# Performance work log

Measured on AMD Instinct MI355X. Metric: run time of the kernel, lower is better.

Reference implementation:

```python
import jax, jax.numpy as jnp
import numpy as np

N = 50000      # nodes
E = 400000     # edges
HID = 128      # hidden size
H = 8          # heads
HS = HID // H  # head size = 16
TN = 8         # node types
R = 8          # relation (edge) types
L = 2          # layers
OUT = 128
EPS = 1e-5
SQRT_D = float(np.sqrt(HS))


def setup_inputs() -> dict:
    key = jax.random.key(0)
    ks = jax.random.split(key, 12)
    s = 1.0 / np.sqrt(HID)
    sh = 1.0 / np.sqrt(HS)
    return {
        "x": jax.random.normal(ks[0], (N, HID), jnp.float32),
        "edge_index": jax.random.randint(ks[1], (2, E), 0, N, dtype=jnp.int32),
        "ntype": jax.random.randint(ks[2], (N,), 0, TN, dtype=jnp.int32),
        "etype": jax.random.randint(ks[3], (E,), 0, R, dtype=jnp.int32),
        "Wk": jax.random.normal(ks[4], (L, TN, HID, HID), jnp.float32) * s,
        "Wq": jax.random.normal(ks[5], (L, TN, HID, HID), jnp.float32) * s,
        "Wv": jax.random.normal(ks[6], (L, TN, HID, HID), jnp.float32) * s,
        "Wa": jax.random.normal(ks[7], (L, TN, HID, HID), jnp.float32) * s,
        "pri": jnp.ones((L, H, R), jnp.float32),
        "Watt": jax.random.normal(ks[8], (L, H, R, HS, HS), jnp.float32) * sh,
        "Wmsg": jax.random.normal(ks[9], (L, H, R, HS, HS), jnp.float32) * sh,
        "skip": jnp.ones((L, TN), jnp.float32),
        "ln_g": jnp.ones((L, HID), jnp.float32),
        "ln_b": jnp.zeros((L, HID), jnp.float32),
        "Wff": jax.random.normal(ks[10], (HID, OUT), jnp.float32) * s,
        "bff": jnp.zeros((OUT,), jnp.float32),
    }


def typed_linear(x, types, W):
    """x:(M,din), types:(M,), W:(T,din,dout) -> (M,dout); y = x @ W[type]."""
    out = jnp.zeros((x.shape[0], W.shape[-1]), x.dtype)
    for t in range(W.shape[0]):
        out = out + jnp.where((types == t)[:, None], x @ W[t], 0.0)
    return out


def rel_apply(h, etype, W):
    """h:(E,H,hs), etype:(E,), W:(H,R,hs,hs) -> (E,H,hs); per-head, per-relation linear."""
    out = jnp.zeros_like(h)
    for r in range(W.shape[1]):
        out = out + jnp.where((etype == r)[:, None, None],
                              jnp.einsum('ehi,hio->eho', h, W[:, r]), 0.0)
    return out


def gt_layer(x, src, dst, ntype, etype, Wk, Wq, Wv, Wa, pri, Watt, Wmsg, skip, g, b):
    n = x.shape[0]
    k = typed_linear(x, ntype, Wk).reshape(n, H, HS)
    q = typed_linear(x, ntype, Wq).reshape(n, H, HS)
    v = typed_linear(x, ntype, Wv).reshape(n, H, HS)
    k_j, q_i, v_j = k[src], q[dst], v[src]          # (E,H,hs)
    kw = rel_apply(k_j, etype, Watt)                # relation-specific key transform
    a = (kw * q_i).sum(-1) * pri[:, etype].T / SQRT_D  # (E,H)
    # scatter softmax over destination nodes
    amax = jax.ops.segment_max(a, dst, num_segments=n)
    ex = jnp.exp(a - amax[dst])
    den = jax.ops.segment_sum(ex, dst, num_segments=n)
    alpha = ex / (den[dst] + 1e-16)
    m = rel_apply(v_j, etype, Wmsg)                 # relation-specific message
    agg = jax.ops.segment_sum(alpha[..., None] * m, dst, num_segments=n)
    out = jax.nn.silu(typed_linear(agg.reshape(n, HID), ntype, Wa))
    al = jax.nn.sigmoid(skip[ntype])[:, None]
    out = out * al + x * (1.0 - al)                 # gated residual (in==hid)
    mu = out.mean(-1, keepdims=True)
    var = ((out - mu) ** 2).mean(-1, keepdims=True)
    return (out - mu) / jnp.sqrt(var + EPS) * g + b


def reference(x, edge_index, ntype, etype, Wk, Wq, Wv, Wa, pri, Watt, Wmsg,
              skip, ln_g, ln_b, Wff, bff):
    src, dst = edge_index[0], edge_index[1]
    emb = x
    for l in range(L):
        emb = gt_layer(emb, src, dst, ntype, etype, Wk[l], Wq[l], Wv[l], Wa[l],
                       pri[l], Watt[l], Wmsg[l], skip[l], ln_g[l], ln_b[l])
    return emb @ Wff + bff
```

## Files before the change

kernel.cpp:

```cpp
#include <hip/hip_runtime.h>
#include <hip/hip_bf16.h>
#include <math.h>

#define N_NODES 50000
#define N_EDGES 400000
#define HID 128
#define NH 8
#define HS 16
#define TN 8
#define NR 8
#define TILE 32
#define MAXTILES 1571
#define PERM_SZ (MAXTILES * TILE)
#define SCAN_BLKS ((N_NODES + 255) / 256)
#define NB 3125
#define TPBMAX 26
#define CAP 288

typedef __attribute__((ext_vector_type(8))) short bf16x8;
typedef __attribute__((ext_vector_type(4))) float f32x4;

__device__ __forceinline__ unsigned short f2bf(float f) {
    __hip_bfloat16 h = __float2bfloat16(f);
    return *reinterpret_cast<unsigned short*>(&h);
}
__device__ __forceinline__ float bf2f(unsigned short u) {
    return __uint_as_float((unsigned)u << 16);
}

__global__ void hist_kernel(const int* __restrict__ ntype, int* __restrict__ cnt) {
    __shared__ int l[TN];
    if (threadIdx.x < TN) l[threadIdx.x] = 0;
    __syncthreads();
    int i = blockIdx.x * 256 + threadIdx.x;
    if (i < N_NODES) atomicAdd(&l[ntype[i]], 1);
    __syncthreads();
    if (threadIdx.x < TN) atomicAdd(&cnt[threadIdx.x], l[threadIdx.x]);
}
__global__ void scan_kernel(const int* __restrict__ cnt, int* __restrict__ cursor) {
    if (threadIdx.x == 0 && blockIdx.x == 0) {
        int acc = 0;
        for (int t = 0; t < TN; ++t) {
            cursor[t] = acc;
            acc += ((cnt[t] + TILE - 1) / TILE) * TILE;
        }
    }
}
__global__ void scatter_kernel(const int* __restrict__ ntype, int* __restrict__ cursor,
                               int* __restrict__ perm) {
    __shared__ int lcnt[TN], lbase[TN];
    if (threadIdx.x < TN) lcnt[threadIdx.x] = 0;
    __syncthreads();
    int i = blockIdx.x * 256 + threadIdx.x;
    int t = 0, off = 0;
    if (i < N_NODES) {
        t = ntype[i];
        off = atomicAdd(&lcnt[t], 1);
    }
    __syncthreads();
    if (threadIdx.x < TN)
        lbase[threadIdx.x] = atomicAdd(&cursor[threadIdx.x], lcnt[threadIdx.x]);
    __syncthreads();
    if (i < N_NODES) perm[lbase[t] + off] = i;
}

__global__ void hist_dst_kernel(const int* __restrict__ dst, int* __restrict__ cnt) {
    int e = blockIdx.x * 256 + threadIdx.x;
    if (e < N_EDGES) atomicAdd(&cnt[dst[e]], 1);
}
__global__ void scan_block_kernel(const int* __restrict__ cnt, int* __restrict__ excl,
                                  int* __restrict__ bsum) {
    __shared__ int s[256];
    int tid = threadIdx.x;
    int i = blockIdx.x * 256 + tid;
    int v = (i < N_NODES) ? cnt[i] : 0;
    s[tid] = v;
    __syncthreads();
    for (int off = 1; off < 256; off <<= 1) {
        int t = (tid >= off) ? s[tid - off] : 0;
        __syncthreads();
        s[tid] += t;
        __syncthreads();
    }
    if (i < N_NODES) excl[i] = s[tid] - v;
    if (tid == 255) bsum[blockIdx.x] = s[255];
}
__global__ void scan_top_kernel(int* __restrict__ bsum) {
    __shared__ int s[256];
    int tid = threadIdx.x;
    int v = (tid < SCAN_BLKS) ? bsum[tid] : 0;
    s[tid] = v;
    __syncthreads();
    for (int off = 1; off < 256; off <<= 1) {
        int t = (tid >= off) ? s[tid - off] : 0;
        __syncthreads();
        s[tid] += t;
        __syncthreads();
    }
    if (tid < SCAN_BLKS) bsum[tid] = s[tid] - v;
}
__global__ void scan_add_kernel(int* __restrict__ excl, const int* __restrict__ bsum,
                                int* __restrict__ cursor) {
    int i = blockIdx.x * 256 + threadIdx.x;
    if (i < N_NODES) {
        int v = excl[i] + bsum[blockIdx.x];
        excl[i] = v;
        cursor[i] = v;
    }
}
__global__ void csr_scatter_kernel(const int* __restrict__ src, const int* __restrict__ dst,
                                   const int* __restrict__ etype, int* __restrict__ cur_dst,
                                   int* __restrict__ csr_sd, int* __restrict__ csr_et) {
    int e = blockIdx.x * 256 + threadIdx.x;
    if (e < N_EDGES) {
        int p = atomicAdd(&cur_dst[dst[e]], 1);
        csr_sd[p] = src[e] | (dst[e] << 16);
        csr_et[p] = etype[e];
    }
}

__global__ void btile_build(const int* __restrict__ row_ptr,
                            const int* __restrict__ csr_sd, const int* __restrict__ csr_et,
                            int* __restrict__ btile_sd, int* __restrict__ btile_lp,
                            int* __restrict__ btile_r, int* __restrict__ ntb) {
    int b = blockIdx.x;
    int lane = threadIdx.x;
    int p0 = row_ptr[b * 16];
    int p1 = (b == NB - 1) ? N_EDGES : row_ptr[b * 16 + 16];
    int cnt = 0;
    if (lane < 8) {
        for (int p = p0; p < p1; ++p) cnt += (csr_et[p] == lane);
    }
    int tiles = (cnt + 15) >> 4;
    int pre = 0, total = 0;
    for (int k = 0; k < 8; ++k) {
        int tk = __shfl(tiles, k);
        if (k < lane) pre += tk;
        total += tk;
    }
    if (lane == 0) ntb[b] = total;
    if (lane < 8) {
        int tbase = b * TPBMAX + pre;
        for (int t = 0; t < tiles; ++t) btile_r[tbase + t] = lane;
        int off = 0;
        for (int p = p0; p < p1; ++p) {
            if (csr_et[p] == lane) {
                int idx = (tbase + (off >> 4)) * 16 + (off & 15);
                btile_sd[idx] = csr_sd[p];
                btile_lp[idx] = p - p0;
                ++off;
            }
        }
        for (; off < tiles * 16; ++off) {
            int idx = (tbase + (off >> 4)) * 16 + (off & 15);
            btile_sd[idx] = 0;
            btile_lp[idx] = CAP;
        }
    }
}

__global__ void wconv_kernel(const float* __restrict__ W, unsigned short* __restrict__ out) {
    int mat = blockIdx.x >> 3, seg = blockIdx.x & 7;
    const float* w = W + (size_t)mat * HID * HID;
    unsigned short* o = out + (size_t)mat * HID * HID;
#pragma unroll
    for (int c = 0; c < 8; ++c) {
        int idx = seg * 2048 + c * 256 + threadIdx.x;
        int i = idx >> 7, j = idx & 127;
        o[j * HID + i] = f2bf(w[idx]);
    }
}
__global__ void wsmall_conv(const float* __restrict__ W, const float* __restrict__ pri,
                            unsigned short* __restrict__ out) {
    int blk = blockIdx.x;
    int tid = threadIdx.x;
    int i = tid >> 4, o = tid & 15;
    float s = pri ? pri[blk] * 0.25f : 1.f;
    out[blk * 256 + o * 16 + i] = f2bf(W[blk * 256 + i * 16 + o] * s);
}

__global__ __launch_bounds__(256) void gemm3_mfma(
    const float* __restrict__ x, const int* __restrict__ perm, const int* __restrict__ ntype,
    const unsigned short* __restrict__ WkT, const unsigned short* __restrict__ WqT,
    const unsigned short* __restrict__ WvT,
    unsigned short* __restrict__ Kb, unsigned short* __restrict__ Qb,
    unsigned short* __restrict__ Vb) {
    __shared__ unsigned short xs[TILE][HID + 8];
    __shared__ int nodes[TILE];
    int tid = threadIdx.x;
    if (tid < TILE) nodes[tid] = perm[blockIdx.x * TILE + tid];
    __syncthreads();
    if (nodes[0] < 0) return;
    int t = ntype[nodes[0]];
#pragma unroll
    for (int c = 0; c < 4; ++c) {
        int v = tid + c * 256;
        int ns = v >> 5, ii = (v & 31) * 4;
        int node = nodes[ns];
        float4 val = (node >= 0) ? *(const float4*)(x + (size_t)node * HID + ii)
                                 : make_float4(0.f, 0.f, 0.f, 0.f);
        uint2 pk;
        pk.x = (unsigned)f2bf(val.x) | ((unsigned)f2bf(val.y) << 16);
        pk.y = (unsigned)f2bf(val.z) | ((unsigned)f2bf(val.w) << 16);
        *(uint2*)&xs[ns][ii] = pk;
    }
    __syncthreads();
    int wv = tid >> 6, lane = tid & 63;
    int lrow = lane & 15, lk = lane >> 4;
    bf16x8 af[2][4];
#pragma unroll
    for (int rt = 0; rt < 2; ++rt)
#pragma unroll
        for (int kk = 0; kk < 4; ++kk)
            af[rt][kk] = *(const bf16x8*)&xs[rt * 16 + lrow][kk * 32 + lk * 8];
    size_t woff = (size_t)t * HID * HID + (size_t)lrow * HID + lk * 8;
#pragma unroll
    for (int pp = 0; pp < 6; ++pp) {
        int p = wv * 6 + pp;
        int mat = p >> 3, ct = p & 7;
        const unsigned short* wb =
            (mat == 0 ? WkT : (mat == 1 ? WqT : WvT)) + woff + (size_t)ct * 16 * HID;
        unsigned short* ob = (mat == 0) ? Kb : (mat == 1 ? Qb : Vb);
        f32x4 a0 = {0.f, 0.f, 0.f, 0.f}, a1 = {0.f, 0.f, 0.f, 0.f};
#pragma unroll
        for (int kk = 0; kk < 4; ++kk) {
            bf16x8 bfr = *(const bf16x8*)(wb + kk * 32);
            a0 = __builtin_amdgcn_mfma_f32_16x16x32_bf16(af[0][kk], bfr, a0, 0, 0, 0);
            a1 = __builtin_amdgcn_mfma_f32_16x16x32_bf16(af[1][kk], bfr, a1, 0, 0, 0);
        }
        int col = ct * 16 + lrow;
#pragma unroll
        for (int q = 0; q < 4; ++q) {
            int r0 = lk * 4 + q;
            int n0 = nodes[r0], n1 = nodes[16 + r0];
            if (n0 >= 0) ob[(size_t)n0 * HID + col] = f2bf(a0[q]);
            if (n1 >= 0) ob[(size_t)n1 * HID + col] = f2bf(a1[q]);
        }
    }
}

__global__ __launch_bounds__(256) void gemm1_mfma(
    const float* __restrict__ x, const int* __restrict__ perm, const int* __restrict__ ntype,
    const unsigned short* __restrict__ Wt, const float* __restrict__ bias,
    float* __restrict__ out) {
    __shared__ unsigned short xs[TILE][HID + 8];
    __shared__ int nodes[TILE];
    int tid = threadIdx.x;
    if (tid < TILE) {
        int n;
        if (perm) n = perm[blockIdx.x * TILE + tid];
        else { n = blockIdx.x * TILE + tid; if (n >= N_NODES) n = -1; }
        nodes[tid] = n;
    }
    __syncthreads();
    if (nodes[0] < 0) return;
    int t = perm ? ntype[nodes[0]] : 0;
#pragma unroll
    for (int c = 0; c < 4; ++c) {
        int v = tid + c * 256;
        int ns = v >> 5, ii = (v & 31) * 4;
        int node = nodes[ns];
        float4 val = (node >= 0) ? *(const float4*)(x + (size_t)node * HID + ii)
                                 : make_float4(0.f, 0.f, 0.f, 0.f);
        uint2 pk;
        pk.x = (unsigned)f2bf(val.x) | ((unsigned)f2bf(val.y) << 16);
        pk.y = (unsigned)f2bf(val.z) | ((unsigned)f2bf(val.w) << 16);
        *(uint2*)&xs[ns][ii] = pk;
    }
    __syncthreads();
    int wv = tid >> 6, lane = tid & 63;
    int lrow = lane & 15, lk = lane >> 4;
    bf16x8 af[2][4];
#pragma unroll
    for (int rt = 0; rt < 2; ++rt)
#pragma unroll
        for (int kk = 0; kk < 4; ++kk)
            af[rt][kk] = *(const bf16x8*)&xs[rt * 16 + lrow][kk * 32 + lk * 8];
    const unsigned short* wb0 = Wt + (size_t)t * HID * HID + (size_t)lrow * HID + lk * 8;
#pragma unroll
    for (int pp = 0; pp < 2; ++pp) {
        int ct = wv * 2 + pp;
        const unsigned short* wb = wb0 + (size_t)ct * 16 * HID;
        f32x4 a0 = {0.f, 0.f, 0.f, 0.f}, a1 = {0.f, 0.f, 0.f, 0.f};
#pragma unroll
        for (int kk = 0; kk < 4; ++kk) {
            bf16x8 bfr = *(const bf16x8*)(wb + kk * 32);
            a0 = __builtin_amdgcn_mfma_f32_16x16x32_bf16(af[0][kk], bfr, a0, 0, 0, 0);
            a1 = __builtin_amdgcn_mfma_f32_16x16x32_bf16(af[1][kk], bfr, a1, 0, 0, 0);
        }
        float bv = bias ? bias[ct * 16 + lrow] : 0.f;
#pragma unroll
        for (int q = 0; q < 4; ++q) {
            int r0 = lk * 4 + q;
            int n0 = nodes[r0], n1 = nodes[16 + r0];
            if (n0 >= 0) out[(size_t)n0 * HID + ct * 16 + lrow] = a0[q] + bv;
            if (n1 >= 0) out[(size_t)n1 * HID + ct * 16 + lrow] = a1[q] + bv;
        }
    }
}

__global__ __launch_bounds__(256) void gemm1_ln_mfma(
    const unsigned short* __restrict__ aggb, const int* __restrict__ perm,
    const int* __restrict__ ntype, const unsigned short* __restrict__ Wt,
    const float* __restrict__ xin, const float* __restrict__ skip,
    const float* __restrict__ g, const float* __restrict__ b, float* __restrict__ xout) {
    __shared__ unsigned short xs[TILE][HID + 8];
    __shared__ int nodes[TILE];
    __shared__ float psum[TILE][4], psq[TILE][4];
    __shared__ float mu_s[TILE], rv_s[TILE];
    int tid = threadIdx.x;
    if (tid < TILE) nodes[tid] = perm[blockIdx.x * TILE + tid];
    __syncthreads();
    if (nodes[0] < 0) return;
    int t = ntype[nodes[0]];
#pragma unroll
    for (int c = 0; c < 4; ++c) {
        int v = tid + c * 256;
        int ns = v >> 5, ii = (v & 31) * 4;
        int node = nodes[ns];
        uint2 pk = make_uint2(0u, 0u);
        if (node >= 0) pk = *(const uint2*)(aggb + (size_t)node * HID + ii);
        *(uint2*)&xs[ns][ii] = pk;
    }
    __syncthreads();
    int wv = tid >> 6, lane = tid & 63;
    int lrow = lane & 15, lk = lane >> 4;
    bf16x8 af[2][4];
#pragma unroll
    for (int rt = 0; rt < 2; ++rt)
#pragma unroll
        for (int kk = 0; kk < 4; ++kk)
            af[rt][kk] = *(const bf16x8*)&xs[rt * 16 + lrow][kk * 32 + lk * 8];
    const unsigned short* wb0 = Wt + (size_t)t * HID * HID + (size_t)lrow * HID + lk * 8;
    float al = 1.f / (1.f + __expf(-skip[t]));
    float om = 1.f - al;
    float ov[2][2][4];
#pragma unroll
    for (int pp = 0; pp < 2; ++pp) {
        int ct = wv * 2 + pp;
        const unsigned short* wb = wb0 + (size_t)ct * 16 * HID;
        f32x4 a0 = {0.f, 0.f, 0.f, 0.f}, a1 = {0.f, 0.f, 0.f, 0.f};
#pragma unroll
        for (int kk = 0; kk < 4; ++kk) {
            bf16x8 bfr = *(const bf16x8*)(wb + kk * 32);
            a0 = __builtin_amdgcn_mfma_f32_16x16x32_bf16(af[0][kk], bfr, a0, 0, 0, 0);
            a1 = __builtin_amdgcn_mfma_f32_16x16x32_bf16(af[1][kk], bfr, a1, 0, 0, 0);
        }
        int col = ct * 16 + lrow;
#pragma unroll
        for (int q = 0; q < 4; ++q) {
            int n0 = nodes[lk * 4 + q], n1 = nodes[16 + lk * 4 + q];
            float s0 = a0[q] / (1.f + __expf(-a0[q]));
            float s1 = a1[q] / (1.f + __expf(-a1[q]));
            float x0 = (n0 >= 0) ? xin[(size_t)n0 * HID + col] : 0.f;
            float x1 = (n1 >= 0) ? xin[(size_t)n1 * HID + col] : 0.f;
            ov[pp][0][q] = s0 * al + x0 * om;
            ov[pp][1][q] = s1 * al + x1 * om;
        }
    }
#pragma unroll
    for (int half = 0; half < 2; ++half)
#pragma unroll
        for (int q = 0; q < 4; ++q) {
            float s = ov[0][half][q] + ov[1][half][q];
            float s2 = ov[0][half][q] * ov[0][half][q] + ov[1][half][q] * ov[1][half][q];
            s += __shfl_xor(s, 1); s += __shfl_xor(s, 2);
            s += __shfl_xor(s, 4); s += __shfl_xor(s, 8);
            s2 += __shfl_xor(s2, 1); s2 += __shfl_xor(s2, 2);
            s2 += __shfl_xor(s2, 4); s2 += __shfl_xor(s2, 8);
            if (lrow == 0) {
                int nd = half * 16 + lk * 4 + q;
                psum[nd][wv] = s;
                psq[nd][wv] = s2;
            }
        }
    __syncthreads();
    if (tid < TILE) {
        float s = psum[tid][0] + psum[tid][1] + psum[tid][2] + psum[tid][3];
        float s2 = psq[tid][0] + psq[tid][1] + psq[tid][2] + psq[tid][3];
        float mu = s * (1.f / HID);
        float var = s2 * (1.f / HID) - mu * mu;
        mu_s[tid] = mu;
        rv_s[tid] = rsqrtf(fmaxf(var, 0.f) + 1e-5f);
    }
    __syncthreads();
#pragma unroll
    for (int pp = 0; pp < 2; ++pp) {
        int col = (wv * 2 + pp) * 16 + lrow;
        float gg = g[col], bb = b[col];
#pragma unroll
        for (int q = 0; q < 4; ++q) {
            int i0 = lk * 4 + q, i1 = 16 + lk * 4 + q;
            int n0 = nodes[i0], n1 = nodes[i1];
            if (n0 >= 0) xout[(size_t)n0 * HID + col] = (ov[pp][0][q] - mu_s[i0]) * rv_s[i0] * gg + bb;
            if (n1 >= 0) xout[(size_t)n1 * HID + col] = (ov[pp][1][q] - mu_s[i1]) * rv_s[i1] * gg + bb;
        }
    }
}

__global__ __launch_bounds__(512) void fused_attn_kernel(
    const unsigned short* __restrict__ Kb, const unsigned short* __restrict__ Vb,
    const unsigned short* __restrict__ Qb,
    const int* __restrict__ row_ptr, const int* __restrict__ deg,
    const int* __restrict__ btile_sd, const int* __restrict__ btile_lp,
    const int* __restrict__ btile_r, const int* __restrict__ ntb,
    const unsigned short* __restrict__ WattT, const unsigned short* __restrict__ WmsgT,
    unsigned short* __restrict__ aggb) {
    __shared__ unsigned short smg[CAP + 1][72];
    __shared__ float ssc[CAP + 1][4];
    int b = blockIdx.x;
    int wv = threadIdx.x >> 6, lane = threadIdx.x & 63;
    int ecol = lane & 15, lk = lane >> 4;
    int nt = ntb[b];
    int p0 = row_ptr[b * 16];
    const bf16x8 zz = {0, 0, 0, 0, 0, 0, 0, 0};

#pragma unroll
    for (int pass = 0; pass < 2; ++pass) {
        int hbase = pass * 4;
        for (int t = wv; t < nt; t += 8) {
            int ti = b * TPBMAX + t;
            int r = btile_r[ti];
            int sd = btile_sd[ti * 16 + ecol];
            int lp = btile_lp[ti * 16 + ecol];
            int s = sd & 0xFFFF, dd = ((unsigned)sd >> 16);
#pragma unroll
            for (int hh = 0; hh < 4; ++hh) {
                int h = hbase + hh;
                bf16x8 bk = zz, bv = zz, aa = zz, am = zz;
                if (lk < 2) {
                    bk = *(const bf16x8*)(Kb + (size_t)s * HID + h * HS + lk * 8);
                    bv = *(const bf16x8*)(Vb + (size_t)s * HID + h * HS + lk * 8);
                    int wo = ((h * NR + r) * 16 + ecol) * 16 + lk * 8;
                    aa = *(const bf16x8*)(WattT + wo);
                    am = *(const bf16x8*)(WmsgT + wo);
                }
                f32x4 ck = {0.f, 0.f, 0.f, 0.f}, cm = {0.f, 0.f, 0.f, 0.f};
                ck = __builtin_amdgcn_mfma_f32_16x16x32_bf16(aa, bk, ck, 0, 0, 0);
                cm = __builtin_amdgcn_mfma_f32_16x16x32_bf16(am, bv, cm, 0, 0, 0);
                uint2 qraw = *(const uint2*)(Qb + (size_t)dd * HID + h * HS + lk * 4);
                float q0 = __uint_as_float(qraw.x << 16);
                float q1 = __uint_as_float(qraw.x & 0xffff0000u);
                float q2 = __uint_as_float(qraw.y << 16);
                float q3 = __uint_as_float(qraw.y & 0xffff0000u);
                float xsc = ck[0] * q0 + ck[1] * q1 + ck[2] * q2 + ck[3] * q3;
                xsc += __shfl_xor(xsc, 16);
                xsc += __shfl_xor(xsc, 32);
                if (lk == 0) ssc[lp][hh] = xsc;
                uint2 pk2;
                pk2.x = (unsigned)f2bf(cm[0]) | ((unsigned)f2bf(cm[1]) << 16);
                pk2.y = (unsigned)f2bf(cm[2]) | ((unsigned)f2bf(cm[3]) << 16);
                *(uint2*)&smg[lp][hh * 16 + lk * 4] = pk2;
            }
        }
        __syncthreads();
        int h2 = lane >> 4, o = lane & 15;
#pragma unroll
        for (int i = 0; i < 2; ++i) {
            int d = b * 16 + wv * 2 + i;
            int lo = row_ptr[d] - p0;
            int dg = deg[d];
            float m = -INFINITY, den = 0.f, acc = 0.f;
            for (int e = 0; e < dg; ++e) {
                int lp = lo + e;
                float a = ssc[lp][h2];
                float gv = bf2f(smg[lp][h2 * 16 + o]);
                float mn = fmaxf(m, a);
                float scale = __expf(m - mn);
                float ex = __expf(a - mn);
                den = den * scale + ex;
                acc = acc * scale + ex * gv;
                m = mn;
            }
            aggb[(size_t)d * HID + (hbase + h2) * HS + o] = f2bf(acc / (den + 1e-16f));
        }
        __syncthreads();
    }
}

extern "C" void kernel_launch(void* const* d_in, const int* in_sizes, int n_in,
                              void* d_out, int out_size, void* d_ws, size_t ws_size,
                              hipStream_t stream) {
    const float* x     = (const float*)d_in[0];
    const int*   eidx  = (const int*)d_in[1];
    const int*   ntype = (const int*)d_in[2];
    const int*   etype = (const int*)d_in[3];
    const float* Wk    = (const float*)d_in[4];
    const float* Wq    = (const float*)d_in[5];
    const float* Wv    = (const float*)d_in[6];
    const float* Wa    = (const float*)d_in[7];
    const float* pri   = (const float*)d_in[8];
    const float* Watt  = (const float*)d_in[9];
    const float* Wmsg  = (const float*)d_in[10];
    const float* skip  = (const float*)d_in[11];
    const float* ln_g  = (const float*)d_in[12];
    const float* ln_b  = (const float*)d_in[13];
    const float* Wff   = (const float*)d_in[14];
    const float* bff   = (const float*)d_in[15];
    const int* src = eidx;
    const int* dst = eidx + N_EDGES;

    char* ws = (char*)d_ws;
    size_t szN = (size_t)N_NODES * HID * sizeof(float);
    float* embA = (float*)(ws);
    unsigned short* AGGb = (unsigned short*)(ws + szN);
    char*  kvq  = ws + 2 * szN;
    unsigned short* Kbf = (unsigned short*)kvq;
    unsigned short* Vbf = (unsigned short*)(kvq + (size_t)N_NODES * HID * 2);
    unsigned short* Qbf = (unsigned short*)(kvq + 2 * (size_t)N_NODES * HID * 2);
    float* l1out = (float*)kvq;
    char*  p    = kvq + 3 * (size_t)N_NODES * HID * 2;
    int* perm    = (int*)p;  p += (size_t)PERM_SZ * 4;
    int* cnt     = (int*)p;  p += TN * 4;
    int* cursor  = (int*)p;  p += TN * 4;
    int* row_ptr = (int*)p;  p += (size_t)N_NODES * 4;
    int* cnt_dst = (int*)p;  p += (size_t)N_NODES * 4;
    int* cur_dst = (int*)p;  p += (size_t)N_NODES * 4;
    int* bsum    = (int*)p;  p += 256 * 4;
    int* csr_sd  = (int*)p;  p += (size_t)N_EDGES * 4;
    int* csr_et  = (int*)p;  p += (size_t)N_EDGES * 4;
    int* btile_sd = (int*)p; p += (size_t)NB * TPBMAX * 16 * 4;
    int* btile_lp = (int*)p; p += (size_t)NB * TPBMAX * 16 * 4;
    int* btile_r  = (int*)p; p += (size_t)NB * TPBMAX * 4;
    int* ntb      = (int*)p; p += (size_t)NB * 4;
    size_t wmat = (size_t)HID * HID;
    unsigned short* WkT  = (unsigned short*)p;  p += 2 * TN * wmat * 2;
    unsigned short* WqT  = (unsigned short*)p;  p += 2 * TN * wmat * 2;
    unsigned short* WvT  = (unsigned short*)p;  p += 2 * TN * wmat * 2;
    unsigned short* WaT  = (unsigned short*)p;  p += 2 * TN * wmat * 2;
    unsigned short* WffT = (unsigned short*)p;  p += wmat * 2;
    unsigned short* WattT = (unsigned short*)p; p += 2 * 64 * 256 * 2;
    unsigned short* WmsgT = (unsigned short*)p; p += 2 * 64 * 256 * 2;

    wconv_kernel<<<2 * TN * 8, 256, 0, stream>>>(Wk, WkT);
    wconv_kernel<<<2 * TN * 8, 256, 0, stream>>>(Wq, WqT);
    wconv_kernel<<<2 * TN * 8, 256, 0, stream>>>(Wv, WvT);
    wconv_kernel<<<2 * TN * 8, 256, 0, stream>>>(Wa, WaT);
    wconv_kernel<<<8, 256, 0, stream>>>(Wff, WffT);
    wsmall_conv<<<128, 256, 0, stream>>>(Watt, pri, WattT);
    wsmall_conv<<<128, 256, 0, stream>>>(Wmsg, nullptr, WmsgT);

    hipMemsetAsync(cnt, 0, TN * 4, stream);
    hipMemsetAsync(perm, 0xFF, (size_t)PERM_SZ * 4, stream);
    hist_kernel<<<(N_NODES + 255) / 256, 256, 0, stream>>>(ntype, cnt);
    scan_kernel<<<1, 64, 0, stream>>>(cnt, cursor);
    scatter_kernel<<<(N_NODES + 255) / 256, 256, 0, stream>>>(ntype, cursor, perm);

    hipMemsetAsync(cnt_dst, 0, (size_t)N_NODES * 4, stream);
    hist_dst_kernel<<<(N_EDGES + 255) / 256, 256, 0, stream>>>(dst, cnt_dst);
    scan_block_kernel<<<SCAN_BLKS, 256, 0, stream>>>(cnt_dst, row_ptr, bsum);
    scan_top_kernel<<<1, 256, 0, stream>>>(bsum);
    scan_add_kernel<<<SCAN_BLKS, 256, 0, stream>>>(row_ptr, bsum, cur_dst);
    csr_scatter_kernel<<<(N_EDGES + 255) / 256, 256, 0, stream>>>(src, dst, etype, cur_dst,
                                                                  csr_sd, csr_et);
    btile_build<<<NB, 64, 0, stream>>>(row_ptr, csr_sd, csr_et,
                                       btile_sd, btile_lp, btile_r, ntb);

    for (int l = 0; l < 2; ++l) {
        const float* xin = l ? embA : x;
        float* xout = l ? l1out : embA;
        const float* skip_l = skip + (size_t)l * TN;
        const float* g_l    = ln_g + (size_t)l * HID;
        const float* b_l    = ln_b + (size_t)l * HID;
        const unsigned short* WkT_l = WkT + (size_t)l * TN * wmat;
        const unsigned short* WqT_l = WqT + (size_t)l * TN * wmat;
        const unsigned short* WvT_l = WvT + (size_t)l * TN * wmat;
        const unsigned short* WaT_l = WaT + (size_t)l * TN * wmat;
        const unsigned short* WattT_l = WattT + (size_t)l * 64 * 256;
        const unsigned short* WmsgT_l = WmsgT + (size_t)l * 64 * 256;

        gemm3_mfma<<<MAXTILES, 256, 0, stream>>>(xin, perm, ntype, WkT_l, WqT_l, WvT_l,
                                                 Kbf, Qbf, Vbf);
        fused_attn_kernel<<<NB, 512, 0, stream>>>(Kbf, Vbf, Qbf, row_ptr, cnt_dst,
                                                  btile_sd, btile_lp, btile_r, ntb,
                                                  WattT_l, WmsgT_l, AGGb);
        gemm1_ln_mfma<<<MAXTILES, 256, 0, stream>>>(AGGb, perm, ntype, WaT_l, xin,
                                                    skip_l, g_l, b_l, xout);
    }
    gemm1_mfma<<<(N_NODES + TILE - 1) / TILE, 256, 0, stream>>>(l1out, nullptr, ntype, WffT,
                                                                bff, (float*)d_out);
}
```

Baseline: 438.8 us.

## Merge weight-conversion launches, split attention work per tile-head, repad LDS

The five weight-transpose launches become one kernel that picks its source matrix from the block index, which cuts launch overhead. In the fused attention kernel, each (tile, head) pair is now a separate work item spread across the waves, rather than each wave handling all four heads of a tile. The goal is better load balance when a block has few tiles. LDS row pitches change to 68 shorts and 5 floats to alter the bank-conflict pattern, at the cost of reloading tile metadata once per head.

```diff
diff --git a/kernel.cpp b/kernel.cpp
--- a/kernel.cpp
+++ b/kernel.cpp
@@ -16,6 +16,8 @@
 #define NB 3125
 #define TPBMAX 26
 #define CAP 288
+#define MPITCH 68
+#define SPITCH 5
 
 typedef __attribute__((ext_vector_type(8))) short bf16x8;
 typedef __attribute__((ext_vector_type(4))) float f32x4;
@@ -159,10 +161,27 @@
     }
 }
 
-__global__ void wconv_kernel(const float* __restrict__ W, unsigned short* __restrict__ out) {
-    int mat = blockIdx.x >> 3, seg = blockIdx.x & 7;
-    const float* w = W + (size_t)mat * HID * HID;
-    unsigned short* o = out + (size_t)mat * HID * HID;
+__global__ void wconv_all_kernel(const float* __restrict__ Wk, const float* __restrict__ Wq,
+                                 const float* __restrict__ Wv, const float* __restrict__ Wa,
+                                 const float* __restrict__ Wff,
+                                 unsigned short* __restrict__ WkT, unsigned short* __restrict__ WqT,
+                                 unsigned short* __restrict__ WvT, unsigned short* __restrict__ WaT,
+                                 unsigned short* __restrict__ WffT) {
+    int blk = blockIdx.x;
+    int m16 = blk >> 3;
+    int seg = blk & 7;
+    const float* w;
+    unsigned short* o;
+    if (m16 < 64) {
+        int grp = m16 >> 4, mat = m16 & 15;
+        const float* Wsrc = grp == 0 ? Wk : (grp == 1 ? Wq : (grp == 2 ? Wv : Wa));
+        unsigned short* Wdst = grp == 0 ? WkT : (grp == 1 ? WqT : (grp == 2 ? WvT : WaT));
+        w = Wsrc + (size_t)mat * HID * HID;
+        o = Wdst + (size_t)mat * HID * HID;
+    } else {
+        w = Wff;
+        o = WffT;
+    }
 #pragma unroll
     for (int c = 0; c < 8; ++c) {
         int idx = seg * 2048 + c * 256 + threadIdx.x;
@@ -406,8 +425,8 @@
     const int* __restrict__ btile_r, const int* __restrict__ ntb,
     const unsigned short* __restrict__ WattT, const unsigned short* __restrict__ WmsgT,
     unsigned short* __restrict__ aggb) {
-    __shared__ unsigned short smg[CAP + 1][72];
-    __shared__ float ssc[CAP + 1][4];
+    __shared__ unsigned short smg[CAP + 1][MPITCH];
+    __shared__ float ssc[CAP + 1][SPITCH];
     int b = blockIdx.x;
     int wv = threadIdx.x >> 6, lane = threadIdx.x & 63;
     int ecol = lane & 15, lk = lane >> 4;
@@ -418,40 +437,39 @@
 #pragma unroll
     for (int pass = 0; pass < 2; ++pass) {
         int hbase = pass * 4;
-        for (int t = wv; t < nt; t += 8) {
+        int nitems = nt * 4;
+        for (int it = wv; it < nitems; it += 8) {
+            int t = it >> 2, hh = it & 3;
+            int h = hbase + hh;
             int ti = b * TPBMAX + t;
             int r = btile_r[ti];
             int sd = btile_sd[ti * 16 + ecol];
             int lp = btile_lp[ti * 16 + ecol];
             int s = sd & 0xFFFF, dd = ((unsigned)sd >> 16);
-#pragma unroll
-            for (int hh = 0; hh < 4; ++hh) {
-                int h = hbase + hh;
-                bf16x8 bk = zz, bv = zz, aa = zz, am = zz;
-                if (lk < 2) {
-                    bk = *(const bf16x8*)(Kb + (size_t)s * HID + h * HS + lk * 8);
-                    bv = *(const bf16x8*)(Vb + (size_t)s * HID + h * HS + lk * 8);
-                    int wo = ((h * NR + r) * 16 + ecol) * 16 + lk * 8;
-                    aa = *(const bf16x8*)(WattT + wo);
-                    am = *(const bf16x8*)(WmsgT + wo);
-                }
-                f32x4 ck = {0.f, 0.f, 0.f, 0.f}, cm = {0.f, 0.f, 0.f, 0.f};
-                ck = __builtin_amdgcn_mfma_f32_16x16x32_bf16(aa, bk, ck, 0, 0, 0);
-                cm = __builtin_amdgcn_mfma_f32_16x16x32_bf16(am, bv, cm, 0, 0, 0);
-                uint2 qraw = *(const uint2*)(Qb + (size_t)dd * HID + h * HS + lk * 4);
-                float q0 = __uint_as_float(qraw.x << 16);
-                float q1 = __uint_as_float(qraw.x & 0xffff0000u);
-                float q2 = __uint_as_float(qraw.y << 16);
-                float q3 = __uint_as_float(qraw.y & 0xffff0000u);
-                float xsc = ck[0] * q0 + ck[1] * q1 + ck[2] * q2 + ck[3] * q3;
-                xsc += __shfl_xor(xsc, 16);
-                xsc += __shfl_xor(xsc, 32);
-                if (lk == 0) ssc[lp][hh] = xsc;
-                uint2 pk2;
-                pk2.x = (unsigned)f2bf(cm[0]) | ((unsigned)f2bf(cm[1]) << 16);
-                pk2.y = (unsigned)f2bf(cm[2]) | ((unsigned)f2bf(cm[3]) << 16);
-                *(uint2*)&smg[lp][hh * 16 + lk * 4] = pk2;
+            bf16x8 bk = zz, bv = zz, aa = zz, am = zz;
+            if (lk < 2) {
+                bk = *(const bf16x8*)(Kb + (size_t)s * HID + h * HS + lk * 8);
+                bv = *(const bf16x8*)(Vb + (size_t)s * HID + h * HS + lk * 8);
+                int wo = ((h * NR + r) * 16 + ecol) * 16 + lk * 8;
+                aa = *(const bf16x8*)(WattT + wo);
+                am = *(const bf16x8*)(WmsgT + wo);
             }
+            f32x4 ck = {0.f, 0.f, 0.f, 0.f}, cm = {0.f, 0.f, 0.f, 0.f};
+            ck = __builtin_amdgcn_mfma_f32_16x16x32_bf16(aa, bk, ck, 0, 0, 0);
+            cm = __builtin_amdgcn_mfma_f32_16x16x32_bf16(am, bv, cm, 0, 0, 0);
+            uint2 qraw = *(const uint2*)(Qb + (size_t)dd * HID + h * HS + lk * 4);
+            float q0 = __uint_as_float(qraw.x << 16);
+            float q1 = __uint_as_float(qraw.x & 0xffff0000u);
+            float q2 = __uint_as_float(qraw.y << 16);
+            float q3 = __uint_as_float(qraw.y & 0xffff0000u);
+            float xsc = ck[0] * q0 + ck[1] * q1 + ck[2] * q2 + ck[3] * q3;
+            xsc += __shfl_xor(xsc, 16);
+            xsc += __shfl_xor(xsc, 32);
+            if (lk == 0) ssc[lp][hh] = xsc;
+            uint2 pk2;
+            pk2.x = (unsigned)f2bf(cm[0]) | ((unsigned)f2bf(cm[1]) << 16);
+            pk2.y = (unsigned)f2bf(cm[2]) | ((unsigned)f2bf(cm[3]) << 16);
+            *(uint2*)&smg[lp][hh * 16 + lk * 4] = pk2;
         }
         __syncthreads();
         int h2 = lane >> 4, o = lane & 15;
@@ -532,11 +550,8 @@
     unsigned short* WattT = (unsigned short*)p; p += 2 * 64 * 256 * 2;
     unsigned short* WmsgT = (unsigned short*)p; p += 2 * 64 * 256 * 2;
 
-    wconv_kernel<<<2 * TN * 8, 256, 0, stream>>>(Wk, WkT);
-    wconv_kernel<<<2 * TN * 8, 256, 0, stream>>>(Wq, WqT);
-    wconv_kernel<<<2 * TN * 8, 256, 0, stream>>>(Wv, WvT);
-    wconv_kernel<<<2 * TN * 8, 256, 0, stream>>>(Wa, WaT);
-    wconv_kernel<<<8, 256, 0, stream>>>(Wff, WffT);
+    wconv_all_kernel<<<65 * 8, 256, 0, stream>>>(Wk, Wq, Wv, Wa, Wff,
+                                                 WkT, WqT, WvT, WaT, WffT);
     wsmall_conv<<<128, 256, 0, stream>>>(Watt, pri, WattT);
     wsmall_conv<<<128, 256, 0, stream>>>(Wmsg, nullptr, WmsgT);
 
```

Result: slower. 459.9 us (+4.8%).
